# Optimization experiments

Hardware: AMD Instinct MI355X
Metric: run time of the kernel (lower is better)

The kernel has to match this reference:

```python
import jax, jax.numpy as jnp
import numpy as np

B, CIN, H, W = 2, 32, 64, 64
COUT, K, PAD = 32, 3, 1
KK = K * K
PRED_W = COUT * CIN * KK  # 9216 dynamic-weight channels
PRED_OUT = PRED_W + COUT  # + per-pixel bias
EPS = 1e-12


def setup_inputs() -> dict:
    key = jax.random.key(0)
    k1, k2 = jax.random.split(key)
    x = jax.random.normal(k1, (B, CIN, H, W), dtype=jnp.float32)
    # 1x1-conv predictor weights (Conv2d(in_ch, pred_out, 1)), fan-in scaled
    Wp = jax.random.normal(k2, (PRED_OUT, CIN), dtype=jnp.float32) / np.sqrt(CIN).astype(np.float32)
    bp = jnp.zeros((PRED_OUT,), dtype=jnp.float32)
    return {"x": x, "Wp": Wp, "bp": bp}


def _unfold3x3(x):
    # F.unfold with k=3, pad=1, stride=1, dilation=1 -> (B, Cin, 9, L), c slowest then (kh, kw)
    xp = jnp.pad(x, ((0, 0), (0, 0), (PAD, PAD), (PAD, PAD)))
    patches = jnp.stack(
        [xp[:, :, i:i + H, j:j + W] for i in range(K) for j in range(K)], axis=2
    )  # (B, Cin, 9, H, W)
    return patches.reshape(B, CIN, KK, H * W)


def _l2norm(v, axis):
    n = jnp.sqrt(jnp.sum(v * v, axis=axis, keepdims=True))
    return v / jnp.maximum(n, EPS)


def reference(x, Wp, bp):
    L = H * W
    patches = _unfold3x3(x)  # (B, Cin, 9, L)
    # 1x1 conv predictor (stride=1 path -> operates on x directly)
    pred = jnp.einsum('oc,bchw->bohw', Wp, x) + bp[None, :, None, None]  # (B, PRED_OUT, H, W)
    dyn_w = pred[:, :PRED_W].reshape(B, COUT, CIN, KK, L)
    dyn_b = pred[:, PRED_W:].reshape(B, COUT, L)
    # norm_pred: L2-normalize over Cin axis, then over k*k axis
    dyn_w = _l2norm(dyn_w, axis=2)
    dyn_w = _l2norm(dyn_w, axis=3)
    out = jnp.einsum('bockl,bckl->bol', dyn_w, patches) + dyn_b  # (B, Cout, L)
    return out.reshape(B, COUT, H, W)
```

## Files before the change

### kernel.cpp

```cpp
#include <hip/hip_runtime.h>

#define TPB 256

typedef __attribute__((ext_vector_type(8))) short short8;
typedef __attribute__((ext_vector_type(4))) float f32x4;

__device__ __forceinline__ unsigned f2bf_pk(float a, float b) {
  return ((__float_as_uint(a) + 0x8000u) >> 16) | ((__float_as_uint(b) + 0x8000u) & 0xffff0000u);
}
__device__ __forceinline__ float bflo(unsigned v) { return __uint_as_float(v << 16); }
__device__ __forceinline__ float bfhi(unsigned v) { return __uint_as_float(v & 0xffff0000u); }

__device__ __forceinline__ void dma16(const void* g, void* l) {
  __builtin_amdgcn_global_load_lds(
      (const __attribute__((address_space(1))) unsigned*)g,
      (__attribute__((address_space(3))) unsigned*)l, 16, 0, 0);
}

__device__ __forceinline__ float swz16_add(float v) {
  int t = __builtin_amdgcn_ds_swizzle(__float_as_int(v), 0x401F);
  return v + __int_as_float(t);
}

__global__ void prep_kernel(const float* __restrict__ Wp, unsigned* __restrict__ Wq) {
  int idx = blockIdx.x * blockDim.x + threadIdx.x;
  if (idx >= 32 * 18 * 64 * 4) return;
  int j2   = idx & 3;
  int lane = (idx >> 2) & 63;
  int rt   = (idx >> 8) % 18;
  int o    = (idx >> 8) / 18;
  int m16 = lane & 15, kq = lane >> 4;
  int row = o * 288 + (m16 >> 2) * 72 + rt * 4 + (m16 & 3);
  const float* src = Wp + row * 32 + kq * 8 + j2 * 2;
  Wq[idx] = f2bf_pk(src[0], src[1]);
}

template <bool USE_WQ>
__global__ __launch_bounds__(TPB, 4) void dppc10_kernel(
    const float* __restrict__ x, const float* __restrict__ Wp,
    const float* __restrict__ bp, const unsigned* __restrict__ Wq,
    float* __restrict__ out) {
  __shared__ __align__(16) unsigned short xrow2[3 * 66 * 40];
  __shared__ __align__(16) char wqbuf[18432];

  const int tid = threadIdx.x;
  const int bid = blockIdx.x;
  const int og  = bid & 7;
  const int t   = bid >> 3;
  const int b   = t >> 6;
  const int h   = t & 63;

  const char* wq_g = (const char*)Wq + (size_t)(og * 4) * 18432;

  if (USE_WQ) {
    for (int c = tid; c < 1152; c += TPB)
      dma16(wq_g + c * 16, wqbuf + c * 16);
  }

  for (int i = tid; i < 120; i += TPB) {
    int p = i / 20, w = i % 20;
    ((unsigned*)xrow2)[(((p >> 1) * 66 + ((p & 1) ? 65 : 0)) * 20) + w] = 0;
  }
  for (int i = tid; i < 1536; i += TPB) {
    int px_ = i & 63, c4 = (i >> 6) & 7, r = i >> 9;
    int hh = h - 1 + r;
    unsigned w0 = 0, w1 = 0;
    if ((unsigned)hh < 64u) {
      const float* xp = x + ((b * 32 + c4 * 4) * 64 + hh) * 64 + px_;
      float f0 = xp[0], f1 = xp[4096], f2 = xp[8192], f3 = xp[12288];
      w0 = f2bf_pk(f0, f1);
      w1 = f2bf_pk(f2, f3);
    }
    uint2* dst = (uint2*)&xrow2[(r * 66 + 1 + px_) * 40 + c4 * 4];
    *dst = make_uint2(w0, w1);
  }
  __syncthreads();

  const int lane = tid & 63;
  const int wv   = tid >> 6;
  const int m16  = lane & 15, kq = lane >> 4;
  const int px   = wv * 16 + m16;

#pragma unroll 1
  for (int oo = 0; oo < 4; ++oo) {
    const int o = og * 4 + oo;
    const float* bp_o = bp + og * 1152 + oo * 288;

    const short8 bfrag = *(const short8*)&xrow2[(66 + 1 + px) * 40 + kq * 8];

    f32x4 acc[18];
    if (USE_WQ) {
#pragma unroll
      for (int rt = 0; rt < 18; ++rt) {
        const short8 a = *(const short8*)(wqbuf + (rt * 64 + lane) * 16);
        const f32x4 bb = *(const f32x4*)(bp_o + kq * 72 + rt * 4);
        acc[rt] = __builtin_amdgcn_mfma_f32_16x16x32_bf16(a, bfrag, bb, 0, 0, 0);
      }
    } else {
      const float* ab = Wp + (o * 288 + (m16 >> 2) * 72 + (m16 & 3)) * 32 + kq * 8;
#pragma unroll
      for (int rt = 0; rt < 18; ++rt) {
        const float* ap = ab + rt * 4 * 32;
        float4 a0 = *(const float4*)ap;
        float4 a1 = *(const float4*)(ap + 4);
        union { short8 v; unsigned u[4]; } af;
        af.u[0] = f2bf_pk(a0.x, a0.y);
        af.u[1] = f2bf_pk(a0.z, a0.w);
        af.u[2] = f2bf_pk(a1.x, a1.y);
        af.u[3] = f2bf_pk(a1.z, a1.w);
        const f32x4 bb = *(const f32x4*)(bp_o + kq * 72 + rt * 4);
        acc[rt] = __builtin_amdgcn_mfma_f32_16x16x32_bf16(af.v, bfrag, bb, 0, 0, 0);
      }
    }

    if (USE_WQ && oo < 3) {
      __syncthreads();
      const char* g = wq_g + (size_t)(oo + 1) * 18432;
      for (int c = tid; c < 1152; c += TPB)
        dma16(g + c * 16, wqbuf + c * 16);
    }

    float rinv[9];
#pragma unroll
    for (int kk = 0; kk < 9; ++kk) rinv[kk] = 0.f;
#pragma unroll
    for (int c8 = 0; c8 < 8; ++c8)
#pragma unroll
      for (int kk = 0; kk < 9; ++kk) {
        const int idx = c8 * 9 + kk;
        const float v = acc[idx >> 2][idx & 3];
        rinv[kk] += v * v;
      }
#pragma unroll
    for (int kk = 0; kk < 9; ++kk) {
      float s = swz16_add(rinv[kk]);
      s += __shfl_xor(s, 32);
      rinv[kk] = rsqrtf(fmaxf(s, 1e-24f));
    }

    float s2[8], dot[8];
#pragma unroll
    for (int c8 = 0; c8 < 8; ++c8) { s2[c8] = 0.f; dot[c8] = 0.f; }
#pragma unroll
    for (int kk = 0; kk < 9; ++kk) {
      const int kh = kk / 3, kw = kk - kh * 3;
      const uint4 tp = *(const uint4*)&xrow2[(kh * 66 + kw + px) * 40 + kq * 8];
      const float rv = rinv[kk];
#pragma unroll
      for (int c8 = 0; c8 < 8; ++c8) {
        const int idx = c8 * 9 + kk;
        const float tv = acc[idx >> 2][idx & 3] * rv;
        s2[c8] += tv * tv;
        const unsigned wd = ((const unsigned*)&tp)[c8 >> 1];
        const float pv = (c8 & 1) ? bfhi(wd) : bflo(wd);
        dot[c8] += tv * pv;
      }
    }

    const float4 wb0 = *(const float4*)(Wp + (9216 + o) * 32 + kq * 8);
    const float4 wb1 = *(const float4*)(Wp + (9216 + o) * 32 + kq * 8 + 4);
    const uint4 tc = *(const uint4*)&xrow2[(66 + 1 + px) * 40 + kq * 8];
    float oacc = 0.f;
#pragma unroll
    for (int c8 = 0; c8 < 8; ++c8) {
      oacc += rsqrtf(fmaxf(s2[c8], 1e-24f)) * dot[c8];
      const unsigned wd = ((const unsigned*)&tc)[c8 >> 1];
      const float xc = (c8 & 1) ? bfhi(wd) : bflo(wd);
      const float wbv = (c8 < 4) ? ((const float*)&wb0)[c8] : ((const float*)&wb1)[c8 - 4];
      oacc += wbv * xc;
    }
    oacc = swz16_add(oacc);
    oacc += __shfl_xor(oacc, 32);
    if (kq == 0)
      out[((b * 32 + o) * 64 + h) * 64 + px] = oacc + bp[9216 + o];

    if (oo < 3) __syncthreads();
  }
}

extern "C" void kernel_launch(void* const* d_in, const int* in_sizes, int n_in,
                              void* d_out, int out_size, void* d_ws, size_t ws_size,
                              hipStream_t stream) {
  const float* x  = (const float*)d_in[0];
  const float* Wp = (const float*)d_in[1];
  const float* bp = (const float*)d_in[2];
  float* out = (float*)d_out;
  const size_t wq_bytes = (size_t)32 * 18 * 64 * 8 * 2;
  if (ws_size >= wq_bytes) {
    prep_kernel<<<576, 256, 0, stream>>>(Wp, (unsigned*)d_ws);
    dppc10_kernel<true><<<1024, TPB, 0, stream>>>(x, Wp, bp, (const unsigned*)d_ws, out);
  } else {
    dppc10_kernel<false><<<1024, TPB, 0, stream>>>(x, Wp, bp, nullptr, out);
  }
}
```

Measured before the change: 80.73 us.

## Drop weight prep kernel and LDS staging; load fp32 weights directly per wave

Removes the separate prep kernel that pre-swizzled Wp into bf16 and the per-iteration global_load_lds staging of those weights into shared memory. Each wave now reads fp32 weights straight from global memory and converts them to bf16 in registers. This drops one kernel launch and all intra-loop __syncthreads. It also hoists the B fragment out of the output loop and folds the bias-weight dot product into the centre-tap iteration. The cost is twice the global weight bytes per block, plus conversion ALU work on every load.

```diff
diff --git a/kernel.cpp b/kernel.cpp
--- a/kernel.cpp
+++ b/kernel.cpp
@@ -11,37 +11,15 @@
 __device__ __forceinline__ float bflo(unsigned v) { return __uint_as_float(v << 16); }
 __device__ __forceinline__ float bfhi(unsigned v) { return __uint_as_float(v & 0xffff0000u); }
 
-__device__ __forceinline__ void dma16(const void* g, void* l) {
-  __builtin_amdgcn_global_load_lds(
-      (const __attribute__((address_space(1))) unsigned*)g,
-      (__attribute__((address_space(3))) unsigned*)l, 16, 0, 0);
-}
-
 __device__ __forceinline__ float swz16_add(float v) {
   int t = __builtin_amdgcn_ds_swizzle(__float_as_int(v), 0x401F);
   return v + __int_as_float(t);
 }
 
-__global__ void prep_kernel(const float* __restrict__ Wp, unsigned* __restrict__ Wq) {
-  int idx = blockIdx.x * blockDim.x + threadIdx.x;
-  if (idx >= 32 * 18 * 64 * 4) return;
-  int j2   = idx & 3;
-  int lane = (idx >> 2) & 63;
-  int rt   = (idx >> 8) % 18;
-  int o    = (idx >> 8) / 18;
-  int m16 = lane & 15, kq = lane >> 4;
-  int row = o * 288 + (m16 >> 2) * 72 + rt * 4 + (m16 & 3);
-  const float* src = Wp + row * 32 + kq * 8 + j2 * 2;
-  Wq[idx] = f2bf_pk(src[0], src[1]);
-}
-
-template <bool USE_WQ>
-__global__ __launch_bounds__(TPB, 4) void dppc10_kernel(
+__global__ __launch_bounds__(TPB, 4) void dppc11_kernel(
     const float* __restrict__ x, const float* __restrict__ Wp,
-    const float* __restrict__ bp, const unsigned* __restrict__ Wq,
-    float* __restrict__ out) {
+    const float* __restrict__ bp, float* __restrict__ out) {
   __shared__ __align__(16) unsigned short xrow2[3 * 66 * 40];
-  __shared__ __align__(16) char wqbuf[18432];
 
   const int tid = threadIdx.x;
   const int bid = blockIdx.x;
@@ -49,13 +27,6 @@
   const int t   = bid >> 3;
   const int b   = t >> 6;
   const int h   = t & 63;
-
-  const char* wq_g = (const char*)Wq + (size_t)(og * 4) * 18432;
-
-  if (USE_WQ) {
-    for (int c = tid; c < 1152; c += TPB)
-      dma16(wq_g + c * 16, wqbuf + c * 16);
-  }
 
   for (int i = tid; i < 120; i += TPB) {
     int p = i / 20, w = i % 20;
@@ -81,43 +52,27 @@
   const int m16  = lane & 15, kq = lane >> 4;
   const int px   = wv * 16 + m16;
 
+  const short8 bfrag = *(const short8*)&xrow2[(66 + 1 + px) * 40 + kq * 8];
+
 #pragma unroll 1
   for (int oo = 0; oo < 4; ++oo) {
     const int o = og * 4 + oo;
-    const float* bp_o = bp + og * 1152 + oo * 288;
-
-    const short8 bfrag = *(const short8*)&xrow2[(66 + 1 + px) * 40 + kq * 8];
+    const float* bp_o = bp + o * 288;
 
     f32x4 acc[18];
-    if (USE_WQ) {
+    const float* ab = Wp + (o * 288 + (m16 >> 2) * 72 + (m16 & 3)) * 32 + kq * 8;
 #pragma unroll
-      for (int rt = 0; rt < 18; ++rt) {
-        const short8 a = *(const short8*)(wqbuf + (rt * 64 + lane) * 16);
-        const f32x4 bb = *(const f32x4*)(bp_o + kq * 72 + rt * 4);
-        acc[rt] = __builtin_amdgcn_mfma_f32_16x16x32_bf16(a, bfrag, bb, 0, 0, 0);
-      }
-    } else {
-      const float* ab = Wp + (o * 288 + (m16 >> 2) * 72 + (m16 & 3)) * 32 + kq * 8;
-#pragma unroll
-      for (int rt = 0; rt < 18; ++rt) {
-        const float* ap = ab + rt * 4 * 32;
-        float4 a0 = *(const float4*)ap;
-        float4 a1 = *(const float4*)(ap + 4);
-        union { short8 v; unsigned u[4]; } af;
-        af.u[0] = f2bf_pk(a0.x, a0.y);
-        af.u[1] = f2bf_pk(a0.z, a0.w);
-        af.u[2] = f2bf_pk(a1.x, a1.y);
-        af.u[3] = f2bf_pk(a1.z, a1.w);
-        const f32x4 bb = *(const f32x4*)(bp_o + kq * 72 + rt * 4);
-        acc[rt] = __builtin_amdgcn_mfma_f32_16x16x32_bf16(af.v, bfrag, bb, 0, 0, 0);
-      }
-    }
-
-    if (USE_WQ && oo < 3) {
-      __syncthreads();
-      const char* g = wq_g + (size_t)(oo + 1) * 18432;
-      for (int c = tid; c < 1152; c += TPB)
-        dma16(g + c * 16, wqbuf + c * 16);
+    for (int rt = 0; rt < 18; ++rt) {
+      const float* ap = ab + rt * 128;
+      float4 a0 = *(const float4*)ap;
+      float4 a1 = *(const float4*)(ap + 4);
+      union { short8 v; unsigned u[4]; } af;
+      af.u[0] = f2bf_pk(a0.x, a0.y);
+      af.u[1] = f2bf_pk(a0.z, a0.w);
+      af.u[2] = f2bf_pk(a1.x, a1.y);
+      af.u[3] = f2bf_pk(a1.z, a1.w);
+      const f32x4 bb = *(const f32x4*)(bp_o + kq * 72 + rt * 4);
+      acc[rt] = __builtin_amdgcn_mfma_f32_16x16x32_bf16(af.v, bfrag, bb, 0, 0, 0);
     }
 
     float rinv[9];
@@ -138,7 +93,10 @@
       rinv[kk] = rsqrtf(fmaxf(s, 1e-24f));
     }
 
+    const float4 wb0 = *(const float4*)(Wp + (9216 + o) * 32 + kq * 8);
+    const float4 wb1 = *(const float4*)(Wp + (9216 + o) * 32 + kq * 8 + 4);
     float s2[8], dot[8];
+    float bacc = 0.f;
 #pragma unroll
     for (int c8 = 0; c8 < 8; ++c8) { s2[c8] = 0.f; dot[c8] = 0.f; }
 #pragma unroll
@@ -154,27 +112,22 @@
         const unsigned wd = ((const unsigned*)&tp)[c8 >> 1];
         const float pv = (c8 & 1) ? bfhi(wd) : bflo(wd);
         dot[c8] += tv * pv;
+        if (kk == 4) {
+          const float wbv = (c8 < 4) ? ((const float*)&wb0)[c8]
+                                     : ((const float*)&wb1)[c8 - 4];
+          bacc += wbv * pv;
+        }
       }
     }
 
-    const float4 wb0 = *(const float4*)(Wp + (9216 + o) * 32 + kq * 8);
-    const float4 wb1 = *(const float4*)(Wp + (9216 + o) * 32 + kq * 8 + 4);
-    const uint4 tc = *(const uint4*)&xrow2[(66 + 1 + px) * 40 + kq * 8];
-    float oacc = 0.f;
+    float oacc = bacc;
 #pragma unroll
-    for (int c8 = 0; c8 < 8; ++c8) {
+    for (int c8 = 0; c8 < 8; ++c8)
       oacc += rsqrtf(fmaxf(s2[c8], 1e-24f)) * dot[c8];
-      const unsigned wd = ((const unsigned*)&tc)[c8 >> 1];
-      const float xc = (c8 & 1) ? bfhi(wd) : bflo(wd);
-      const float wbv = (c8 < 4) ? ((const float*)&wb0)[c8] : ((const float*)&wb1)[c8 - 4];
-      oacc += wbv * xc;
-    }
     oacc = swz16_add(oacc);
     oacc += __shfl_xor(oacc, 32);
     if (kq == 0)
       out[((b * 32 + o) * 64 + h) * 64 + px] = oacc + bp[9216 + o];
-
-    if (oo < 3) __syncthreads();
   }
 }
 
@@ -185,11 +138,5 @@
   const float* Wp = (const float*)d_in[1];
   const float* bp = (const float*)d_in[2];
   float* out = (float*)d_out;
-  const size_t wq_bytes = (size_t)32 * 18 * 64 * 8 * 2;
-  if (ws_size >= wq_bytes) {
-    prep_kernel<<<576, 256, 0, stream>>>(Wp, (unsigned*)d_ws);
-    dppc10_kernel<true><<<1024, TPB, 0, stream>>>(x, Wp, bp, (const unsigned*)d_ws, out);
-  } else {
-    dppc10_kernel<false><<<1024, TPB, 0, stream>>>(x, Wp, bp, nullptr, out);
-  }
+  dppc11_kernel<<<1024, TPB, 0, stream>>>(x, Wp, bp, out);
 }
```

Result: slower. 177.1 us (+119.4%).
